# Kernel tuning notes

Measured on AMD Instinct MI355X. Metric: run time of the kernel, lower is better.

## Reference

```python
import jax, jax.numpy as jnp
import numpy as np

N_FACTORS = 8
CHANNEL = 4096
EPS = 1e-8


def setup_inputs() -> dict:
    key = jax.random.key(0)
    disen_weight_att = jax.random.normal(key, (N_FACTORS, CHANNEL), dtype=jnp.float32)
    return {"disen_weight_att": disen_weight_att}


def reference(disen_weight_att):
    # Faithful vectorized version of Cul_cor(ind='distance') forward:
    # sum over i<j of DistanceCorrelation(w[i], w[j]).
    x = disen_weight_att                      # [F, C]
    F_, C = x.shape
    sq = x ** 2                               # [F, C]
    # pairwise squared distances per factor: sq_k + sq_l - 2*x_k*x_l  -> [F, C, C]
    d = sq[:, :, None] + sq[:, None, :] - 2.0 * x[:, :, None] * x[:, None, :]
    a = jnp.sqrt(jnp.maximum(d, 0.0) + EPS)   # [F, C, C] distance matrices
    # double centering (a is symmetric, but keep both means for fidelity)
    row_mean = a.mean(axis=2, keepdims=True)  # mean over dim=1 in torch (per row)
    col_mean = a.mean(axis=1, keepdims=True)  # mean over dim=0 in torch (per col)
    tot_mean = a.mean(axis=(1, 2), keepdims=True)
    A = a - col_mean - row_mean + tot_mean    # [F, C, C]
    # all pairwise Frobenius inner products in one GEMM
    Af = A.reshape(F_, C * C)                 # [F, C*C]
    S = (Af @ Af.T) / (C ** 2)                # [F, F]; S[i,j] = (A_i*A_j).sum()/C^2
    dcov = jnp.sqrt(jnp.maximum(S, 0.0) + EPS)
    diag = jnp.diagonal(dcov)                 # dcov_AA per factor
    ratio = dcov / jnp.sqrt(diag[:, None] * diag[None, :] + EPS)
    mask = jnp.triu(jnp.ones((F_, F_), dtype=x.dtype), k=1)  # i < j pairs
    cor = jnp.sum(ratio * mask)
    return cor
```

## Files before the change

kernel.cpp:

```cpp
#include <hip/hip_runtime.h>
#include <math.h>

#define F 8
#define C 4096
#define NPAIR 36
#define EPSF 1e-8f

#define QCH 128
#define NQC (C / QCH)
#define NPG 32
#define NBLK (NPG * NQC)
#define XSROW 132

#define NSB 128
#define SO 116

#define WS_PART (NQC * F * C)
#define WS_GP   (NBLK * 256)

typedef __attribute__((ext_vector_type(8))) short short8v;
typedef __attribute__((ext_vector_type(4))) float f32x4;

__device__ __forceinline__ float wave_reduce(float v) {
    #pragma unroll
    for (int off = 32; off > 0; off >>= 1) v += __shfl_down(v, off, 64);
    return v;
}

__global__ __launch_bounds__(256) void gramrs_kernel(const float* __restrict__ x,
                                                     float* __restrict__ part,
                                                     float* __restrict__ gpart) {
    __shared__ __align__(16) float xs[F * XSROW];
    __shared__ float red[4 * 256];
    const int tid  = threadIdx.x;
    const int lane = tid & 63;
    const int wave = tid >> 6;
    const int pg = blockIdx.x >> 5;
    const int qc = blockIdx.x & 31;
    const int Q0 = qc * QCH;

    {
        const int sf = tid >> 5, si = tid & 31;
        *(float4*)(xs + sf * XSROW + 4 * si) =
            *(const float4*)(x + sf * C + Q0 + 4 * si);
    }

    const int f  = lane & 7;
    const int b  = (lane >> 3) & 1;
    const int hi = (lane >> 4) & 1;
    const int qq = (lane >> 5) & 1;
    const int pgbase = (pg * 4 + wave) * 32;
    const int p0 = pgbase + 16 * b + 8 * hi;

    float xp[8];
    *(float4*)&xp[0] = *(const float4*)(x + f * C + p0);
    *(float4*)&xp[4] = *(const float4*)(x + f * C + p0 + 4);

    union { unsigned u[4]; short8v v; } ind;
    {
        const int col = lane & 15, gg = lane >> 4;
        const int ea  = col - 8 * (gg & 1);
        #pragma unroll
        for (int t = 0; t < 4; ++t) {
            const unsigned lo = (ea == 2 * t)     ? 0x3F80u : 0u;
            const unsigned hb = (ea == 2 * t + 1) ? 0x3F80u : 0u;
            ind.u[t] = lo | (hb << 16);
        }
    }

    f32x4 acc    = {0.f, 0.f, 0.f, 0.f};
    f32x4 acc_rs = {0.f, 0.f, 0.f, 0.f};

    __syncthreads();

    const float* xrow = xs + f * XSROW + 64 * qq;
    #pragma unroll 4
    for (int s4 = 0; s4 < 16; ++s4) {
        const float4 q4 = *(const float4*)(xrow + 4 * s4);
        #pragma unroll
        for (int u = 0; u < 4; ++u) {
            const float xq = (u == 0) ? q4.x : (u == 1) ? q4.y : (u == 2) ? q4.z : q4.w;
            float d[8];
            #pragma unroll
            for (int j = 0; j < 8; ++j) d[j] = xq - xp[j];
            union { unsigned u32[4]; short8v v; } fr;
            #pragma unroll
            for (int t = 0; t < 4; ++t)
                asm("v_cvt_pk_bf16_f32 %0, abs(%1), abs(%2)"
                    : "=v"(fr.u32[t]) : "v"(d[2 * t]), "v"(d[2 * t + 1]));
            acc    = __builtin_amdgcn_mfma_f32_16x16x32_bf16(fr.v, fr.v, acc, 0, 0, 0);
            acc_rs = __builtin_amdgcn_mfma_f32_16x16x32_bf16(fr.v, ind.v, acc_rs, 0, 0, 0);
        }
    }

    {
        const int pslot = lane & 15;
        #pragma unroll
        for (int r = 0; r < 4; ++r) {
            const int row = (lane >> 4) * 4 + r;
            const int ff = row & 7, bb = row >> 3;
            part[(qc * F + ff) * C + (pgbase + 16 * bb + pslot)] = acc_rs[r];
        }
    }

    {
        const int col = lane & 15, r0 = (lane >> 4) * 4;
        #pragma unroll
        for (int r = 0; r < 4; ++r)
            red[wave * 256 + (r0 + r) * 16 + col] = acc[r];
    }
    __syncthreads();
    gpart[blockIdx.x * 256 + tid] =
        red[tid] + red[256 + tid] + red[512 + tid] + red[768 + tid];
}

__global__ __launch_bounds__(256) void sred_kernel(const float* __restrict__ part,
                                                   const float* __restrict__ gpart,
                                                   float* __restrict__ sout) {
    __shared__ float sp[8][F][32];
    const int tid = threadIdx.x;
    const int pi  = tid & 31;
    const int qg  = tid >> 5;
    const int b   = blockIdx.x;
    const int p   = b * 32 + pi;

    float acc[F];
    #pragma unroll
    for (int f = 0; f < F; ++f) acc[f] = 0.0f;
    #pragma unroll
    for (int q4 = 0; q4 < NQC / 8; ++q4) {
        const int qc = qg * (NQC / 8) + q4;
        #pragma unroll
        for (int f = 0; f < F; ++f) acc[f] += part[(qc * F + f) * C + p];
    }
    #pragma unroll
    for (int f = 0; f < F; ++f) sp[qg][f][pi] = acc[f];
    __syncthreads();

    if (tid < 64) {
        float vals[44];
        if (tid < 32) {
            float sv[F];
            #pragma unroll
            for (int f = 0; f < F; ++f) {
                float s = 0.f;
                #pragma unroll
                for (int g2 = 0; g2 < 8; ++g2) s += sp[g2][f][pi];
                sv[f] = s;
            }
            int k = 0;
            #pragma unroll
            for (int i = 0; i < F; ++i)
                #pragma unroll
                for (int j = i; j < F; ++j) { vals[k] = sv[i] * sv[j]; ++k; }
            #pragma unroll
            for (int f2 = 0; f2 < F; ++f2) vals[36 + f2] = sv[f2];
        } else {
            #pragma unroll
            for (int k = 0; k < 44; ++k) vals[k] = 0.f;
        }
        #pragma unroll
        for (int k = 0; k < 44; ++k) vals[k] = wave_reduce(vals[k]);
        if (tid == 0) {
            #pragma unroll
            for (int k = 0; k < 44; ++k) sout[b * SO + k] = vals[k];
        }
    } else if (tid < 64 + 72) {
        const int e  = tid - 64;
        const int eb = (e >= 36) ? e - 36 : e;
        int i = 0, j = eb;
        while (j >= F - i) { j -= F - i; ++i; }
        j += i;
        const int ci = (e >= 36) ? (8 + i) * 16 + (8 + j) : i * 16 + j;
        float s = 0.f;
        #pragma unroll
        for (int r = 0; r < 8; ++r) s += gpart[(b * 8 + r) * 256 + ci];
        sout[b * SO + 44 + e] = s;
    }
}

__global__ __launch_bounds__(256) void finish_kernel(const float* __restrict__ sout,
                                                     float* __restrict__ out) {
    __shared__ float fA[SO][2];
    __shared__ float A[SO];
    const int tid = threadIdx.x;
    if (tid < SO * 2) {
        const int colx = tid >> 1, h = tid & 1;
        float s = 0.f;
        #pragma unroll 16
        for (int i = 0; i < NSB / 2; ++i)
            s += sout[(h * (NSB / 2) + i) * SO + colx];
        fA[colx][h] = s;
    }
    __syncthreads();
    if (tid < SO) A[tid] = fA[tid][0] + fA[tid][1];
    __syncthreads();
    if (tid == 0) {
        const float invC  = 1.0f / (float)C;
        const float invC2 = invC * invC;
        float dcov[NPAIR], diag[F];
        int k = 0;
        for (int i = 0; i < F; ++i)
            for (int j = i; j < F; ++j) {
                const float G = A[44 + k] + A[80 + k];
                const float S = G * invC2 - 2.0f * A[k] * invC2 * invC
                              + (A[36 + i] * invC2) * (A[36 + j] * invC2);
                const float dc = __builtin_amdgcn_sqrtf(fmaxf(S, 0.0f) + EPSF);
                dcov[k] = dc;
                if (i == j) diag[i] = dc;
                ++k;
            }
        float cor = 0.f;
        k = 0;
        for (int i = 0; i < F; ++i)
            for (int j = i; j < F; ++j) {
                if (j > i)
                    cor += dcov[k] * __builtin_amdgcn_rcpf(
                               __builtin_amdgcn_sqrtf(diag[i] * diag[j] + EPSF));
                ++k;
            }
        out[0] = cor;
    }
}

extern "C" void kernel_launch(void* const* d_in, const int* in_sizes, int n_in,
                              void* d_out, int out_size, void* d_ws, size_t ws_size,
                              hipStream_t stream) {
    const float* x = (const float*)d_in[0];
    float* part  = (float*)d_ws;
    float* gpart = part + WS_PART;
    float* sout  = gpart + WS_GP;
    float* out   = (float*)d_out;

    hipLaunchKernelGGL(gramrs_kernel, dim3(NBLK), dim3(256), 0, stream, x, part, gpart);
    hipLaunchKernelGGL(sred_kernel,   dim3(NSB),  dim3(256), 0, stream, part, gpart, sout);
    hipLaunchKernelGGL(finish_kernel, dim3(1),    dim3(256), 0, stream, sout, out);
}
```

Baseline: 70.67 us.

## Fuse finish into reduction kernel via last-block counter; double gram block size

Merges the single-block finish kernel into the reduction kernel. An atomic counter lets the last block to arrive compute the final scalar, which removes one kernel launch and its inter-kernel gap. The gram kernel now runs 512 threads per block, covering two point-groups and sharing one staged x tile, so it launches half as many blocks. The counter is reset by the first gram block each call, which relies on stream ordering and on thread fences for visibility. The larger blocks use more shared memory and may lower occupancy.

```diff
diff --git a/kernel.cpp b/kernel.cpp
--- a/kernel.cpp
+++ b/kernel.cpp
@@ -9,14 +9,15 @@
 #define QCH 128
 #define NQC (C / QCH)
 #define NPG 32
-#define NBLK (NPG * NQC)
+#define NBLK ((NPG / 2) * NQC)
 #define XSROW 132
 
 #define NSB 128
 #define SO 116
 
 #define WS_PART (NQC * F * C)
-#define WS_GP   (NBLK * 256)
+#define WS_GP   (NPG * NQC * 256)
+#define WS_SOUT (NSB * SO)
 
 typedef __attribute__((ext_vector_type(8))) short short8v;
 typedef __attribute__((ext_vector_type(4))) float f32x4;
@@ -27,19 +28,25 @@
     return v;
 }
 
-__global__ __launch_bounds__(256) void gramrs_kernel(const float* __restrict__ x,
+__global__ __launch_bounds__(512) void gramrs_kernel(const float* __restrict__ x,
                                                      float* __restrict__ part,
-                                                     float* __restrict__ gpart) {
+                                                     float* __restrict__ gpart,
+                                                     int* __restrict__ cnt) {
     __shared__ __align__(16) float xs[F * XSROW];
-    __shared__ float red[4 * 256];
+    __shared__ float red[8 * 256];
     const int tid  = threadIdx.x;
     const int lane = tid & 63;
     const int wave = tid >> 6;
-    const int pg = blockIdx.x >> 5;
-    const int qc = blockIdx.x & 31;
-    const int Q0 = qc * QCH;
-
-    {
+    const int half = wave >> 2;
+    const int wv4  = wave & 3;
+    const int pgpair = blockIdx.x >> 5;
+    const int qc     = blockIdx.x & 31;
+    const int pg     = pgpair * 2 + half;
+    const int Q0     = qc * QCH;
+
+    if (blockIdx.x == 0 && tid == 0) *cnt = 0;
+
+    if (tid < 256) {
         const int sf = tid >> 5, si = tid & 31;
         *(float4*)(xs + sf * XSROW + 4 * si) =
             *(const float4*)(x + sf * C + Q0 + 4 * si);
@@ -49,7 +56,7 @@
     const int b  = (lane >> 3) & 1;
     const int hi = (lane >> 4) & 1;
     const int qq = (lane >> 5) & 1;
-    const int pgbase = (pg * 4 + wave) * 32;
+    const int pgbase = (pg * 4 + wv4) * 32;
     const int p0 = pgbase + 16 * b + 8 * hi;
 
     float xp[8];
@@ -110,14 +117,21 @@
             red[wave * 256 + (r0 + r) * 16 + col] = acc[r];
     }
     __syncthreads();
-    gpart[blockIdx.x * 256 + tid] =
-        red[tid] + red[256 + tid] + red[512 + tid] + red[768 + tid];
-}
-
-__global__ __launch_bounds__(256) void sred_kernel(const float* __restrict__ part,
-                                                   const float* __restrict__ gpart,
-                                                   float* __restrict__ sout) {
+    {
+        const int h = tid >> 8, t = tid & 255;
+        const float s = red[(4 * h + 0) * 256 + t] + red[(4 * h + 1) * 256 + t] +
+                        red[(4 * h + 2) * 256 + t] + red[(4 * h + 3) * 256 + t];
+        gpart[((pgpair * 2 + h) * 32 + qc) * 256 + t] = s;
+    }
+}
+
+__global__ __launch_bounds__(256) void sredfin_kernel(const float* __restrict__ part,
+                                                      const float* __restrict__ gpart,
+                                                      float* __restrict__ sout,
+                                                      int* __restrict__ cnt,
+                                                      float* __restrict__ out) {
     __shared__ float sp[8][F][32];
+    __shared__ int isLast;
     const int tid = threadIdx.x;
     const int pi  = tid & 31;
     const int qg  = tid >> 5;
@@ -177,13 +191,16 @@
         for (int r = 0; r < 8; ++r) s += gpart[(b * 8 + r) * 256 + ci];
         sout[b * SO + 44 + e] = s;
     }
-}
-
-__global__ __launch_bounds__(256) void finish_kernel(const float* __restrict__ sout,
-                                                     float* __restrict__ out) {
+
+    __threadfence();
+    __syncthreads();
+    if (tid == 0) isLast = (atomicAdd(cnt, 1) == NSB - 1);
+    __syncthreads();
+    if (!isLast) return;
+    __threadfence();
+
     __shared__ float fA[SO][2];
     __shared__ float A[SO];
-    const int tid = threadIdx.x;
     if (tid < SO * 2) {
         const int colx = tid >> 1, h = tid & 1;
         float s = 0.f;
@@ -230,9 +247,9 @@
     float* part  = (float*)d_ws;
     float* gpart = part + WS_PART;
     float* sout  = gpart + WS_GP;
+    int*   cnt   = (int*)(sout + WS_SOUT);
     float* out   = (float*)d_out;
 
-    hipLaunchKernelGGL(gramrs_kernel, dim3(NBLK), dim3(256), 0, stream, x, part, gpart);
-    hipLaunchKernelGGL(sred_kernel,   dim3(NSB),  dim3(256), 0, stream, part, gpart, sout);
-    hipLaunchKernelGGL(finish_kernel, dim3(1),    dim3(256), 0, stream, sout, out);
-}
+    hipLaunchKernelGGL(gramrs_kernel,  dim3(NBLK), dim3(512), 0, stream, x, part, gpart, cnt);
+    hipLaunchKernelGGL(sredfin_kernel, dim3(NSB),  dim3(256), 0, stream, part, gpart, sout, cnt, out);
+}
```

After: 77.65 us. 9.9% more time.
